# Kernel tuning notes

Measured on AMD Instinct MI355X. Metric: run time of the kernel, lower is better.

Reference implementation:

```python
import jax, jax.numpy as jnp
import numpy as np

N_NODES = 100000
N_EDGES = 1600000
IN_SIZE = 128
HIDDEN = 128
OUT_SIZE = 64


def setup_inputs() -> dict:
    key = jax.random.key(0)
    k = jax.random.split(key, 8)
    feat = jax.random.normal(k[0], (N_NODES, IN_SIZE), dtype=jnp.float32)
    src = jax.random.randint(k[1], (N_EDGES,), 0, N_NODES, dtype=jnp.int32)
    dst = jax.random.randint(k[2], (N_EDGES,), 0, N_NODES, dtype=jnp.int32)
    # fc_neigh weights for the two SAGEConv layers (stored as [in, out])
    W1 = jax.random.normal(k[3], (IN_SIZE, HIDDEN), dtype=jnp.float32) / np.sqrt(IN_SIZE)
    b1 = jnp.zeros((HIDDEN,), dtype=jnp.float32)
    W2 = jax.random.normal(k[4], (HIDDEN, OUT_SIZE), dtype=jnp.float32) / np.sqrt(HIDDEN)
    b2 = jnp.zeros((OUT_SIZE,), dtype=jnp.float32)
    return {"feat": feat, "W1": W1, "b1": b1, "W2": W2, "b2": b2,
            "src": src, "dst": dst}


def _sage_gcn(h, src, dst, W, b):
    # DGL SAGEConv with aggregator_type='gcn':
    #   neigh = segment_sum over incoming edges of src features
    #   h_neigh = (neigh + h_self) / (in_degree + 1)
    #   out = h_neigh @ W + b   (fc_self is not used for 'gcn')
    neigh = jax.ops.segment_sum(h[src], dst, num_segments=N_NODES)  # [N, d]
    deg = jax.ops.segment_sum(jnp.ones((src.shape[0],), dtype=h.dtype), dst,
                              num_segments=N_NODES)                 # [N]
    h_neigh = (neigh + h) / (deg + 1.0)[:, None]
    return h_neigh @ W + b


def reference(feat, W1, b1, W2, b2, src, dst):
    # dropout(p=0.0) is identity; activation between layers only
    h = _sage_gcn(feat, src, dst, W1, b1)
    h = jax.nn.relu(h)
    h = _sage_gcn(h, src, dst, W2, b2)
    return h
```

## Files before the change

### kernel.cpp

```cpp
#include <hip/hip_runtime.h>

#define NNODES 100000
#define NEDGES 1600000
#define BSHIFT 7
#define NB 782
#define CAP 2560
#define EBLOCKS 391
#define GEMM_BLOCKS 1563

typedef _Float16 f16;
typedef _Float16 v4h __attribute__((ext_vector_type(4)));
typedef _Float16 v8h __attribute__((ext_vector_type(8)));
typedef float v4f __attribute__((ext_vector_type(4)));

__global__ __launch_bounds__(256) void init_k(int* __restrict__ bcur,
                                              const float* __restrict__ W1,
                                              f16* __restrict__ W1t,
                                              const float* __restrict__ W2,
                                              f16* __restrict__ W2t) {
    int t = blockIdx.x * 256 + threadIdx.x;
    if (t < NB) bcur[t] = t * CAP;
    int u = t - 1024;
    if (u >= 0) {
        if (u < 128 * 128) {
            int k = u >> 7, n = u & 127;
            W1t[n * 128 + k] = (f16)W1[k * 128 + n];
        } else if (u < 128 * 128 + 128 * 64) {
            int v = u - 128 * 128;
            int k = v >> 6, n = v & 63;
            W2t[n * 128 + k] = (f16)W2[k * 64 + n];
        }
    }
}

__global__ __launch_bounds__(256) void scatter_gemm1(
    const int* __restrict__ src, const int* __restrict__ dst,
    int* __restrict__ bcur, int* __restrict__ ebuf,
    const float* __restrict__ feat, const f16* __restrict__ W1t,
    f16* __restrict__ z1) {
    constexpr int PITCH = 136;
    __shared__ __align__(16) char smem[128 * PITCH * 2];
    int tid = threadIdx.x;

    if (blockIdx.x < EBLOCKS) {
        int* h = (int*)smem;
        int* base_s = ((int*)smem) + 1024;
        for (int i = tid; i < NB; i += 256) h[i] = 0;
        __syncthreads();
        int base = blockIdx.x * 4096;
        int d[16], sv[16];
        for (int k = 0; k < 16; k++) {
            int e = base + k * 256 + tid;
            if (e < NEDGES) {
                d[k] = dst[e];
                sv[k] = src[e];
                atomicAdd(&h[d[k] >> BSHIFT], 1);
            } else {
                d[k] = -1;
            }
        }
        __syncthreads();
        for (int i = tid; i < NB; i += 256) {
            int c = h[i];
            if (c) base_s[i] = atomicAdd(&bcur[i], c);
            h[i] = 0;
        }
        __syncthreads();
        for (int k = 0; k < 16; k++) {
            if (d[k] >= 0) {
                int b = d[k] >> BSHIFT;
                int slot = atomicAdd(&h[b], 1);
                ebuf[base_s[b] + slot] = sv[k] | ((d[k] & 127) << 24);
            }
        }
        return;
    }

    f16* wlds = (f16*)smem;
    for (int c = tid; c < 128 * 16; c += 256) {
        int n = c >> 4;
        int kc = c & 15;
        *(v8h*)&wlds[n * PITCH + kc * 8] = *(const v8h*)&W1t[n * 128 + kc * 8];
    }
    __syncthreads();

    int wave = tid >> 6, lane = tid & 63, quad = lane >> 4, l16 = lane & 15;
    int m0 = (blockIdx.x - EBLOCKS) * 64 + wave * 16;
    if (m0 >= NNODES) return;

    v8h a[4];
    const float* arow = feat + (long)(m0 + l16) * 128 + quad * 8;
#pragma unroll
    for (int kb = 0; kb < 4; kb++) {
        float4 f0 = *(const float4*)(arow + kb * 32);
        float4 f1 = *(const float4*)(arow + kb * 32 + 4);
        v8h t = {(f16)f0.x, (f16)f0.y, (f16)f0.z, (f16)f0.w,
                 (f16)f1.x, (f16)f1.y, (f16)f1.z, (f16)f1.w};
        a[kb] = t;
    }

#pragma unroll
    for (int nt = 0; nt < 8; nt++) {
        v4f acc = {0.f, 0.f, 0.f, 0.f};
        const f16* brow = &wlds[(nt * 16 + l16) * PITCH + quad * 8];
#pragma unroll
        for (int kb = 0; kb < 4; kb++) {
            v8h b = *(const v8h*)(brow + kb * 32);
            acc = __builtin_amdgcn_mfma_f32_16x16x32_f16(a[kb], b, acc, 0, 0, 0);
        }
        int n = nt * 16 + l16;
#pragma unroll
        for (int r = 0; r < 4; r++)
            z1[(long)(m0 + quad * 4 + r) * 128 + n] = (f16)acc[r];
    }
}

__global__ __launch_bounds__(256) void fill_bucket(const int* __restrict__ ebuf,
                                                   const int* __restrict__ bcur,
                                                   int* __restrict__ begs,
                                                   int* __restrict__ ends,
                                                   int* __restrict__ csr) {
    __shared__ int lc[128];
    __shared__ int ls[256];
    int b = blockIdx.x;
    int tid = threadIdx.x;
    if (tid < 128) lc[tid] = 0;
    __syncthreads();
    int ebeg = b * CAP;
    int eend = bcur[b];
    for (int e = ebeg + tid; e < eend; e += 256)
        atomicAdd(&lc[((unsigned)ebuf[e]) >> 24], 1);
    __syncthreads();
    int cnt = (tid < 128) ? lc[tid] : 0;
    ls[tid] = cnt;
    __syncthreads();
    for (int off = 1; off < 256; off <<= 1) {
        int t = (tid >= off) ? ls[tid - off] : 0;
        __syncthreads();
        ls[tid] += t;
        __syncthreads();
    }
    int excl = ls[tid] - cnt;
    int node = (b << BSHIFT) + tid;
    if (tid < 128 && node < NNODES) {
        begs[node] = ebeg + excl;
        ends[node] = ebeg + excl + cnt;
    }
    if (tid < 128) { ls[tid] = excl; lc[tid] = 0; }
    __syncthreads();
    for (int e = ebeg + tid; e < eend; e += 256) {
        int p = ebuf[e];
        int dloc = ((unsigned)p) >> 24;
        int slot = atomicAdd(&lc[dloc], 1);
        csr[ebeg + ls[dloc] + slot] = p & 0xFFFFFF;
    }
}

__global__ __launch_bounds__(1024, 8) void gather128_gemm2(
    const f16* __restrict__ z,
    const int* __restrict__ begs, const int* __restrict__ ends,
    const int* __restrict__ csr,
    const float* __restrict__ b1,
    const f16* __restrict__ W2t,
    f16* __restrict__ z2)
{
    constexpr int PITCH = 136;
    __shared__ f16 w2lds[64 * PITCH];
    __shared__ f16 atile[64 * PITCH];
    int tid = threadIdx.x;

    {
        int n = tid >> 4, kc = tid & 15;
        *(v8h*)&w2lds[n * PITCH + kc * 8] = *(const v8h*)&W2t[n * 128 + kc * 8];
    }

    int wavei = tid >> 6;
    int lane = tid & 63;
    int sub = lane >> 4;
    int c = lane & 15;
    int lnode = wavei * 4 + sub;
    int node = blockIdx.x * 64 + lnode;

    int beg = 0, end = 0;
    if (node < NNODES) { beg = begs[node]; end = ends[node]; }

    const char* zb = (const char*)z;
    unsigned coff = (unsigned)c << 4;

    float af[8];
#pragma unroll
    for (int j = 0; j < 8; j++) af[j] = 0.f;

    if (node < NNODES) {
        v8h sv = *(const v8h*)(zb + ((unsigned)node << 8) + coff);
#pragma unroll
        for (int j = 0; j < 8; j++) af[j] = (float)sv[j];
    }

    int e = beg;
    while (__any(e < end)) {
        v8h u0 = {0,0,0,0,0,0,0,0}, u1 = {0,0,0,0,0,0,0,0};
        v8h u2 = {0,0,0,0,0,0,0,0}, u3 = {0,0,0,0,0,0,0,0};
        v8h u4 = {0,0,0,0,0,0,0,0}, u5 = {0,0,0,0,0,0,0,0};
        v8h u6 = {0,0,0,0,0,0,0,0}, u7 = {0,0,0,0,0,0,0,0};
        if (e     < end) u0 = *(const v8h*)(zb + (((unsigned)csr[e    ]) << 8) + coff);
        if (e + 1 < end) u1 = *(const v8h*)(zb + (((unsigned)csr[e + 1]) << 8) + coff);
        if (e + 2 < end) u2 = *(const v8h*)(zb + (((unsigned)csr[e + 2]) << 8) + coff);
        if (e + 3 < end) u3 = *(const v8h*)(zb + (((unsigned)csr[e + 3]) << 8) + coff);
        if (e + 4 < end) u4 = *(const v8h*)(zb + (((unsigned)csr[e + 4]) << 8) + coff);
        if (e + 5 < end) u5 = *(const v8h*)(zb + (((unsigned)csr[e + 5]) << 8) + coff);
        if (e + 6 < end) u6 = *(const v8h*)(zb + (((unsigned)csr[e + 6]) << 8) + coff);
        if (e + 7 < end) u7 = *(const v8h*)(zb + (((unsigned)csr[e + 7]) << 8) + coff);
        v8h s01 = u0 + u1, s23 = u2 + u3, s45 = u4 + u5, s67 = u6 + u7;
        v8h s03 = s01 + s23, s47 = s45 + s67;
        v8h s = s03 + s47;
#pragma unroll
        for (int j = 0; j < 8; j++) af[j] += (float)s[j];
        e += 8;
    }

    {
        float inv = 1.0f / (float)(end - beg + 1);
        float4 bb0 = ((const float4*)b1)[c * 2];
        float4 bb1 = ((const float4*)b1)[c * 2 + 1];
        v8h o = {(f16)fmaxf(af[0] * inv + bb0.x, 0.f),
                 (f16)fmaxf(af[1] * inv + bb0.y, 0.f),
                 (f16)fmaxf(af[2] * inv + bb0.z, 0.f),
                 (f16)fmaxf(af[3] * inv + bb0.w, 0.f),
                 (f16)fmaxf(af[4] * inv + bb1.x, 0.f),
                 (f16)fmaxf(af[5] * inv + bb1.y, 0.f),
                 (f16)fmaxf(af[6] * inv + bb1.z, 0.f),
                 (f16)fmaxf(af[7] * inv + bb1.w, 0.f)};
        *(v8h*)&atile[lnode * PITCH + c * 8] = o;
    }
    __syncthreads();

    {
        int wr = wavei >> 2, wc = wavei & 3;
        int quad = lane >> 4, l16 = lane & 15;
        const f16* arow = &atile[(wr * 16 + l16) * PITCH + quad * 8];
        const f16* brow = &w2lds[(wc * 16 + l16) * PITCH + quad * 8];
        v4f acc = {0.f, 0.f, 0.f, 0.f};
#pragma unroll
        for (int kb = 0; kb < 4; kb++) {
            v8h av = *(const v8h*)(arow + kb * 32);
            v8h bv = *(const v8h*)(brow + kb * 32);
            acc = __builtin_amdgcn_mfma_f32_16x16x32_f16(av, bv, acc, 0, 0, 0);
        }
        int n = wc * 16 + l16;
        int m0 = blockIdx.x * 64 + wr * 16;
#pragma unroll
        for (int r = 0; r < 4; r++) {
            int row = m0 + quad * 4 + r;
            if (row < NNODES) z2[(long)row * 64 + n] = (f16)acc[r];
        }
    }
}

__global__ __launch_bounds__(256, 8) void gather64(
    const f16* __restrict__ z, const int* __restrict__ begs,
    const int* __restrict__ ends, const int* __restrict__ csr,
    const float* __restrict__ bias, float4* __restrict__ out) {
    int tid = threadIdx.x;
    int lane = tid & 63;
    int c = lane & 7;
    int node = blockIdx.x * 32 + (tid >> 3);

    int beg = begs[node];
    int end = ends[node];

    const char* zb = (const char*)z;
    unsigned coff = (unsigned)c << 4;

    float af[8];
    {
        v8h sv = *(const v8h*)(zb + ((unsigned)node << 7) + coff);
#pragma unroll
        for (int j = 0; j < 8; j++) af[j] = (float)sv[j];
    }

    int e = beg;
    while (__any(e < end)) {
        v8h u0 = {0,0,0,0,0,0,0,0}, u1 = {0,0,0,0,0,0,0,0};
        v8h u2 = {0,0,0,0,0,0,0,0}, u3 = {0,0,0,0,0,0,0,0};
        v8h u4 = {0,0,0,0,0,0,0,0}, u5 = {0,0,0,0,0,0,0,0};
        v8h u6 = {0,0,0,0,0,0,0,0}, u7 = {0,0,0,0,0,0,0,0};
        if (e     < end) u0 = *(const v8h*)(zb + (((unsigned)csr[e    ]) << 7) + coff);
        if (e + 1 < end) u1 = *(const v8h*)(zb + (((unsigned)csr[e + 1]) << 7) + coff);
        if (e + 2 < end) u2 = *(const v8h*)(zb + (((unsigned)csr[e + 2]) << 7) + coff);
        if (e + 3 < end) u3 = *(const v8h*)(zb + (((unsigned)csr[e + 3]) << 7) + coff);
        if (e + 4 < end) u4 = *(const v8h*)(zb + (((unsigned)csr[e + 4]) << 7) + coff);
        if (e + 5 < end) u5 = *(const v8h*)(zb + (((unsigned)csr[e + 5]) << 7) + coff);
        if (e + 6 < end) u6 = *(const v8h*)(zb + (((unsigned)csr[e + 6]) << 7) + coff);
        if (e + 7 < end) u7 = *(const v8h*)(zb + (((unsigned)csr[e + 7]) << 7) + coff);
        v8h s01 = u0 + u1, s23 = u2 + u3, s45 = u4 + u5, s67 = u6 + u7;
        v8h s03 = s01 + s23, s47 = s45 + s67;
        v8h s = s03 + s47;
#pragma unroll
        for (int j = 0; j < 8; j++) af[j] += (float)s[j];
        e += 8;
    }

    {
        float inv = 1.0f / (float)(end - beg + 1);
        float4 b0 = ((const float4*)bias)[c * 2];
        float4 b1v = ((const float4*)bias)[c * 2 + 1];
        out[(long)node * 16 + c * 2] =
            make_float4(af[0] * inv + b0.x, af[1] * inv + b0.y,
                        af[2] * inv + b0.z, af[3] * inv + b0.w);
        out[(long)node * 16 + c * 2 + 1] =
            make_float4(af[4] * inv + b1v.x, af[5] * inv + b1v.y,
                        af[6] * inv + b1v.z, af[7] * inv + b1v.w);
    }
}

extern "C" void kernel_launch(void* const* d_in, const int* in_sizes, int n_in,
                              void* d_out, int out_size, void* d_ws, size_t ws_size,
                              hipStream_t stream) {
    const float* feat = (const float*)d_in[0];
    const float* W1   = (const float*)d_in[1];
    const float* b1   = (const float*)d_in[2];
    const float* W2   = (const float*)d_in[3];
    const float* b2   = (const float*)d_in[4];
    const int*   src  = (const int*)d_in[5];
    const int*   dst  = (const int*)d_in[6];
    float* out = (float*)d_out;

    char* ws = (char*)d_ws;
    int* bcur = (int*)(ws + 0x0000000);
    int* begs = (int*)(ws + 0x0001000);
    int* ends = (int*)(ws + 0x0063000);
    int* csr  = (int*)(ws + 0x00C5000);
    int* ebuf = (int*)(ws + 0x0870000);
    f16* z1   = (f16*)(ws + 0x1100000);
    f16* z2   = (f16*)(ws + 0x2A00000);
    f16* W1t  = (f16*)(ws + 0x3700000);
    f16* W2t  = (f16*)(ws + 0x3710000);

    init_k<<<100, 256, 0, stream>>>(bcur, W1, W1t, W2, W2t);

    scatter_gemm1<<<EBLOCKS + GEMM_BLOCKS, 256, 0, stream>>>(src, dst, bcur, ebuf,
                                                             feat, W1t, z1);

    fill_bucket<<<NB, 256, 0, stream>>>(ebuf, bcur, begs, ends, csr);

    gather128_gemm2<<<1563, 1024, 0, stream>>>(z1, begs, ends, csr, b1, W2t, z2);

    gather64<<<3125, 256, 0, stream>>>(z2, begs, ends, csr, b2, (float4*)out);
}
```

Measured before the change: 247.9 us.

## Quantize intermediate node features to per-row int8 with scales for gathers

The per-node projected features z1 and z2 are now stored as offset-uint8 values with a per-row float scale instead of fp16. The two neighbor-gather kernels dequantize on the fly with fma against the per-row scale and subtract the offset via a running scale sum. This halves the bytes fetched per gathered edge row in the memory-bound gather phases. In exchange it costs an extra scale load per edge, more ALU work, a shared-memory row-max reduction with an added barrier in the second GEMM, and a large loss of numerical precision that may exceed tolerance.

```diff
diff --git a/kernel.cpp b/kernel.cpp
--- a/kernel.cpp
+++ b/kernel.cpp
@@ -9,9 +9,19 @@
 #define GEMM_BLOCKS 1563
 
 typedef _Float16 f16;
-typedef _Float16 v4h __attribute__((ext_vector_type(4)));
 typedef _Float16 v8h __attribute__((ext_vector_type(8)));
 typedef float v4f __attribute__((ext_vector_type(4)));
+
+__device__ inline void acc8(float s, uint2 u, float* a) {
+    a[0] = fmaf(s, (float)(u.x & 0xFF), a[0]);
+    a[1] = fmaf(s, (float)((u.x >> 8) & 0xFF), a[1]);
+    a[2] = fmaf(s, (float)((u.x >> 16) & 0xFF), a[2]);
+    a[3] = fmaf(s, (float)(u.x >> 24), a[3]);
+    a[4] = fmaf(s, (float)(u.y & 0xFF), a[4]);
+    a[5] = fmaf(s, (float)((u.y >> 8) & 0xFF), a[5]);
+    a[6] = fmaf(s, (float)((u.y >> 16) & 0xFF), a[6]);
+    a[7] = fmaf(s, (float)(u.y >> 24), a[7]);
+}
 
 __global__ __launch_bounds__(256) void init_k(int* __restrict__ bcur,
                                               const float* __restrict__ W1,
@@ -37,7 +47,7 @@
     const int* __restrict__ src, const int* __restrict__ dst,
     int* __restrict__ bcur, int* __restrict__ ebuf,
     const float* __restrict__ feat, const f16* __restrict__ W1t,
-    f16* __restrict__ z1) {
+    unsigned char* __restrict__ z1, float* __restrict__ sc1) {
     constexpr int PITCH = 136;
     __shared__ __align__(16) char smem[128 * PITCH * 2];
     int tid = threadIdx.x;
@@ -99,19 +109,36 @@
         a[kb] = t;
     }
 
+    v4f acc[8];
 #pragma unroll
     for (int nt = 0; nt < 8; nt++) {
-        v4f acc = {0.f, 0.f, 0.f, 0.f};
+        v4f c4 = {0.f, 0.f, 0.f, 0.f};
         const f16* brow = &wlds[(nt * 16 + l16) * PITCH + quad * 8];
 #pragma unroll
         for (int kb = 0; kb < 4; kb++) {
             v8h b = *(const v8h*)(brow + kb * 32);
-            acc = __builtin_amdgcn_mfma_f32_16x16x32_f16(a[kb], b, acc, 0, 0, 0);
-        }
-        int n = nt * 16 + l16;
-#pragma unroll
-        for (int r = 0; r < 4; r++)
-            z1[(long)(m0 + quad * 4 + r) * 128 + n] = (f16)acc[r];
+            c4 = __builtin_amdgcn_mfma_f32_16x16x32_f16(a[kb], b, c4, 0, 0, 0);
+        }
+        acc[nt] = c4;
+    }
+
+#pragma unroll
+    for (int r = 0; r < 4; r++) {
+        float m = 0.f;
+#pragma unroll
+        for (int nt = 0; nt < 8; nt++) m = fmaxf(m, fabsf(acc[nt][r]));
+        m = fmaxf(m, __shfl_xor(m, 1));
+        m = fmaxf(m, __shfl_xor(m, 2));
+        m = fmaxf(m, __shfl_xor(m, 4));
+        m = fmaxf(m, __shfl_xor(m, 8));
+        int row = m0 + quad * 4 + r;
+        float rs = (m > 0.f) ? 127.f / m : 0.f;
+        if (l16 == 0) sc1[row] = (m > 0.f) ? m / 127.f : 0.f;
+#pragma unroll
+        for (int nt = 0; nt < 8; nt++) {
+            int qv = (int)rintf(acc[nt][r] * rs) + 128;
+            z1[(long)row * 128 + nt * 16 + l16] = (unsigned char)qv;
+        }
     }
 }
 
@@ -157,22 +184,26 @@
 }
 
 __global__ __launch_bounds__(1024, 8) void gather128_gemm2(
-    const f16* __restrict__ z,
+    const unsigned char* __restrict__ z,
+    const float* __restrict__ sc,
     const int* __restrict__ begs, const int* __restrict__ ends,
     const int* __restrict__ csr,
     const float* __restrict__ b1,
     const f16* __restrict__ W2t,
-    f16* __restrict__ z2)
+    unsigned char* __restrict__ z2,
+    float* __restrict__ sc2)
 {
     constexpr int PITCH = 136;
     __shared__ f16 w2lds[64 * PITCH];
     __shared__ f16 atile[64 * PITCH];
+    __shared__ int rmax[64];
     int tid = threadIdx.x;
 
     {
         int n = tid >> 4, kc = tid & 15;
         *(v8h*)&w2lds[n * PITCH + kc * 8] = *(const v8h*)&W2t[n * 128 + kc * 8];
     }
+    if (tid < 64) rmax[tid] = 0;
 
     int wavei = tid >> 6;
     int lane = tid & 63;
@@ -184,53 +215,55 @@
     int beg = 0, end = 0;
     if (node < NNODES) { beg = begs[node]; end = ends[node]; }
 
-    const char* zb = (const char*)z;
-    unsigned coff = (unsigned)c << 4;
-
-    float af[8];
-#pragma unroll
-    for (int j = 0; j < 8; j++) af[j] = 0.f;
+    unsigned coff = (unsigned)c << 3;
+
+    float a[8];
+#pragma unroll
+    for (int j = 0; j < 8; j++) a[j] = 0.f;
+    float ssum = 0.f;
 
     if (node < NNODES) {
-        v8h sv = *(const v8h*)(zb + ((unsigned)node << 8) + coff);
-#pragma unroll
-        for (int j = 0; j < 8; j++) af[j] = (float)sv[j];
+        float s = sc[node];
+        uint2 u = *(const uint2*)(z + (((unsigned)node) << 7) + coff);
+        ssum += s;
+        acc8(s, u, a);
     }
 
     int e = beg;
     while (__any(e < end)) {
-        v8h u0 = {0,0,0,0,0,0,0,0}, u1 = {0,0,0,0,0,0,0,0};
-        v8h u2 = {0,0,0,0,0,0,0,0}, u3 = {0,0,0,0,0,0,0,0};
-        v8h u4 = {0,0,0,0,0,0,0,0}, u5 = {0,0,0,0,0,0,0,0};
-        v8h u6 = {0,0,0,0,0,0,0,0}, u7 = {0,0,0,0,0,0,0,0};
-        if (e     < end) u0 = *(const v8h*)(zb + (((unsigned)csr[e    ]) << 8) + coff);
-        if (e + 1 < end) u1 = *(const v8h*)(zb + (((unsigned)csr[e + 1]) << 8) + coff);
-        if (e + 2 < end) u2 = *(const v8h*)(zb + (((unsigned)csr[e + 2]) << 8) + coff);
-        if (e + 3 < end) u3 = *(const v8h*)(zb + (((unsigned)csr[e + 3]) << 8) + coff);
-        if (e + 4 < end) u4 = *(const v8h*)(zb + (((unsigned)csr[e + 4]) << 8) + coff);
-        if (e + 5 < end) u5 = *(const v8h*)(zb + (((unsigned)csr[e + 5]) << 8) + coff);
-        if (e + 6 < end) u6 = *(const v8h*)(zb + (((unsigned)csr[e + 6]) << 8) + coff);
-        if (e + 7 < end) u7 = *(const v8h*)(zb + (((unsigned)csr[e + 7]) << 8) + coff);
-        v8h s01 = u0 + u1, s23 = u2 + u3, s45 = u4 + u5, s67 = u6 + u7;
-        v8h s03 = s01 + s23, s47 = s45 + s67;
-        v8h s = s03 + s47;
-#pragma unroll
-        for (int j = 0; j < 8; j++) af[j] += (float)s[j];
+        float s0 = 0.f, s1 = 0.f, s2 = 0.f, s3 = 0.f;
+        float s4 = 0.f, s5 = 0.f, s6 = 0.f, s7 = 0.f;
+        uint2 u0 = make_uint2(0, 0), u1 = make_uint2(0, 0);
+        uint2 u2 = make_uint2(0, 0), u3 = make_uint2(0, 0);
+        uint2 u4 = make_uint2(0, 0), u5 = make_uint2(0, 0);
+        uint2 u6 = make_uint2(0, 0), u7 = make_uint2(0, 0);
+        if (e     < end) { int i = csr[e    ]; s0 = sc[i]; u0 = *(const uint2*)(z + (((unsigned)i) << 7) + coff); }
+        if (e + 1 < end) { int i = csr[e + 1]; s1 = sc[i]; u1 = *(const uint2*)(z + (((unsigned)i) << 7) + coff); }
+        if (e + 2 < end) { int i = csr[e + 2]; s2 = sc[i]; u2 = *(const uint2*)(z + (((unsigned)i) << 7) + coff); }
+        if (e + 3 < end) { int i = csr[e + 3]; s3 = sc[i]; u3 = *(const uint2*)(z + (((unsigned)i) << 7) + coff); }
+        if (e + 4 < end) { int i = csr[e + 4]; s4 = sc[i]; u4 = *(const uint2*)(z + (((unsigned)i) << 7) + coff); }
+        if (e + 5 < end) { int i = csr[e + 5]; s5 = sc[i]; u5 = *(const uint2*)(z + (((unsigned)i) << 7) + coff); }
+        if (e + 6 < end) { int i = csr[e + 6]; s6 = sc[i]; u6 = *(const uint2*)(z + (((unsigned)i) << 7) + coff); }
+        if (e + 7 < end) { int i = csr[e + 7]; s7 = sc[i]; u7 = *(const uint2*)(z + (((unsigned)i) << 7) + coff); }
+        ssum += ((s0 + s1) + (s2 + s3)) + ((s4 + s5) + (s6 + s7));
+        acc8(s0, u0, a); acc8(s1, u1, a); acc8(s2, u2, a); acc8(s3, u3, a);
+        acc8(s4, u4, a); acc8(s5, u5, a); acc8(s6, u6, a); acc8(s7, u7, a);
         e += 8;
     }
 
     {
+        float base = 128.f * ssum;
         float inv = 1.0f / (float)(end - beg + 1);
         float4 bb0 = ((const float4*)b1)[c * 2];
         float4 bb1 = ((const float4*)b1)[c * 2 + 1];
-        v8h o = {(f16)fmaxf(af[0] * inv + bb0.x, 0.f),
-                 (f16)fmaxf(af[1] * inv + bb0.y, 0.f),
-                 (f16)fmaxf(af[2] * inv + bb0.z, 0.f),
-                 (f16)fmaxf(af[3] * inv + bb0.w, 0.f),
-                 (f16)fmaxf(af[4] * inv + bb1.x, 0.f),
-                 (f16)fmaxf(af[5] * inv + bb1.y, 0.f),
-                 (f16)fmaxf(af[6] * inv + bb1.z, 0.f),
-                 (f16)fmaxf(af[7] * inv + bb1.w, 0.f)};
+        v8h o = {(f16)fmaxf((a[0] - base) * inv + bb0.x, 0.f),
+                 (f16)fmaxf((a[1] - base) * inv + bb0.y, 0.f),
+                 (f16)fmaxf((a[2] - base) * inv + bb0.z, 0.f),
+                 (f16)fmaxf((a[3] - base) * inv + bb0.w, 0.f),
+                 (f16)fmaxf((a[4] - base) * inv + bb1.x, 0.f),
+                 (f16)fmaxf((a[5] - base) * inv + bb1.y, 0.f),
+                 (f16)fmaxf((a[6] - base) * inv + bb1.z, 0.f),
+                 (f16)fmaxf((a[7] - base) * inv + bb1.w, 0.f)};
         *(v8h*)&atile[lnode * PITCH + c * 8] = o;
     }
     __syncthreads();
@@ -247,19 +280,35 @@
             v8h bv = *(const v8h*)(brow + kb * 32);
             acc = __builtin_amdgcn_mfma_f32_16x16x32_f16(av, bv, acc, 0, 0, 0);
         }
-        int n = wc * 16 + l16;
-        int m0 = blockIdx.x * 64 + wr * 16;
 #pragma unroll
         for (int r = 0; r < 4; r++) {
-            int row = m0 + quad * 4 + r;
-            if (row < NNODES) z2[(long)row * 64 + n] = (f16)acc[r];
+            float m = fabsf(acc[r]);
+            m = fmaxf(m, __shfl_xor(m, 1));
+            m = fmaxf(m, __shfl_xor(m, 2));
+            m = fmaxf(m, __shfl_xor(m, 4));
+            m = fmaxf(m, __shfl_xor(m, 8));
+            if (l16 == 0) atomicMax(&rmax[wr * 16 + quad * 4 + r], __float_as_int(m));
+        }
+        __syncthreads();
+#pragma unroll
+        for (int r = 0; r < 4; r++) {
+            int lrow = wr * 16 + quad * 4 + r;
+            int row = blockIdx.x * 64 + lrow;
+            if (row < NNODES) {
+                float m = __int_as_float(rmax[lrow]);
+                float rs = (m > 0.f) ? 127.f / m : 0.f;
+                int qv = (int)rintf(acc[r] * rs) + 128;
+                z2[(long)row * 64 + wc * 16 + l16] = (unsigned char)qv;
+                if (l16 == 0 && wc == 0) sc2[row] = (m > 0.f) ? m / 127.f : 0.f;
+            }
         }
     }
 }
 
 __global__ __launch_bounds__(256, 8) void gather64(
-    const f16* __restrict__ z, const int* __restrict__ begs,
-    const int* __restrict__ ends, const int* __restrict__ csr,
+    const unsigned char* __restrict__ z, const float* __restrict__ sc,
+    const int* __restrict__ begs, const int* __restrict__ ends,
+    const int* __restrict__ csr,
     const float* __restrict__ bias, float4* __restrict__ out) {
     int tid = threadIdx.x;
     int lane = tid & 63;
@@ -269,48 +318,53 @@
     int beg = begs[node];
     int end = ends[node];
 
-    const char* zb = (const char*)z;
-    unsigned coff = (unsigned)c << 4;
-
-    float af[8];
+    unsigned coff = (unsigned)c << 3;
+
+    float a[8];
+#pragma unroll
+    for (int j = 0; j < 8; j++) a[j] = 0.f;
+    float ssum = 0.f;
+
     {
-        v8h sv = *(const v8h*)(zb + ((unsigned)node << 7) + coff);
-#pragma unroll
-        for (int j = 0; j < 8; j++) af[j] = (float)sv[j];
+        float s = sc[node];
+        uint2 u = *(const uint2*)(z + (((unsigned)node) << 6) + coff);
+        ssum += s;
+        acc8(s, u, a);
     }
 
     int e = beg;
     while (__any(e < end)) {
-        v8h u0 = {0,0,0,0,0,0,0,0}, u1 = {0,0,0,0,0,0,0,0};
-        v8h u2 = {0,0,0,0,0,0,0,0}, u3 = {0,0,0,0,0,0,0,0};
-        v8h u4 = {0,0,0,0,0,0,0,0}, u5 = {0,0,0,0,0,0,0,0};
-        v8h u6 = {0,0,0,0,0,0,0,0}, u7 = {0,0,0,0,0,0,0,0};
-        if (e     < end) u0 = *(const v8h*)(zb + (((unsigned)csr[e    ]) << 7) + coff);
-        if (e + 1 < end) u1 = *(const v8h*)(zb + (((unsigned)csr[e + 1]) << 7) + coff);
-        if (e + 2 < end) u2 = *(const v8h*)(zb + (((unsigned)csr[e + 2]) << 7) + coff);
-        if (e + 3 < end) u3 = *(const v8h*)(zb + (((unsigned)csr[e + 3]) << 7) + coff);
-        if (e + 4 < end) u4 = *(const v8h*)(zb + (((unsigned)csr[e + 4]) << 7) + coff);
-        if (e + 5 < end) u5 = *(const v8h*)(zb + (((unsigned)csr[e + 5]) << 7) + coff);
-        if (e + 6 < end) u6 = *(const v8h*)(zb + (((unsigned)csr[e + 6]) << 7) + coff);
-        if (e + 7 < end) u7 = *(const v8h*)(zb + (((unsigned)csr[e + 7]) << 7) + coff);
-        v8h s01 = u0 + u1, s23 = u2 + u3, s45 = u4 + u5, s67 = u6 + u7;
-        v8h s03 = s01 + s23, s47 = s45 + s67;
-        v8h s = s03 + s47;
-#pragma unroll
-        for (int j = 0; j < 8; j++) af[j] += (float)s[j];
+        float s0 = 0.f, s1 = 0.f, s2 = 0.f, s3 = 0.f;
+        float s4 = 0.f, s5 = 0.f, s6 = 0.f, s7 = 0.f;
+        uint2 u0 = make_uint2(0, 0), u1 = make_uint2(0, 0);
+        uint2 u2 = make_uint2(0, 0), u3 = make_uint2(0, 0);
+        uint2 u4 = make_uint2(0, 0), u5 = make_uint2(0, 0);
+        uint2 u6 = make_uint2(0, 0), u7 = make_uint2(0, 0);
+        if (e     < end) { int i = csr[e    ]; s0 = sc[i]; u0 = *(const uint2*)(z + (((unsigned)i) << 6) + coff); }
+        if (e + 1 < end) { int i = csr[e + 1]; s1 = sc[i]; u1 = *(const uint2*)(z + (((unsigned)i) << 6) + coff); }
+        if (e + 2 < end) { int i = csr[e + 2]; s2 = sc[i]; u2 = *(const uint2*)(z + (((unsigned)i) << 6) + coff); }
+        if (e + 3 < end) { int i = csr[e + 3]; s3 = sc[i]; u3 = *(const uint2*)(z + (((unsigned)i) << 6) + coff); }
+        if (e + 4 < end) { int i = csr[e + 4]; s4 = sc[i]; u4 = *(const uint2*)(z + (((unsigned)i) << 6) + coff); }
+        if (e + 5 < end) { int i = csr[e + 5]; s5 = sc[i]; u5 = *(const uint2*)(z + (((unsigned)i) << 6) + coff); }
+        if (e + 6 < end) { int i = csr[e + 6]; s6 = sc[i]; u6 = *(const uint2*)(z + (((unsigned)i) << 6) + coff); }
+        if (e + 7 < end) { int i = csr[e + 7]; s7 = sc[i]; u7 = *(const uint2*)(z + (((unsigned)i) << 6) + coff); }
+        ssum += ((s0 + s1) + (s2 + s3)) + ((s4 + s5) + (s6 + s7));
+        acc8(s0, u0, a); acc8(s1, u1, a); acc8(s2, u2, a); acc8(s3, u3, a);
+        acc8(s4, u4, a); acc8(s5, u5, a); acc8(s6, u6, a); acc8(s7, u7, a);
         e += 8;
     }
 
     {
+        float base = 128.f * ssum;
         float inv = 1.0f / (float)(end - beg + 1);
         float4 b0 = ((const float4*)bias)[c * 2];
         float4 b1v = ((const float4*)bias)[c * 2 + 1];
         out[(long)node * 16 + c * 2] =
-            make_float4(af[0] * inv + b0.x, af[1] * inv + b0.y,
-                        af[2] * inv + b0.z, af[3] * inv + b0.w);
+            make_float4((a[0] - base) * inv + b0.x, (a[1] - base) * inv + b0.y,
+                        (a[2] - base) * inv + b0.z, (a[3] - base) * inv + b0.w);
         out[(long)node * 16 + c * 2 + 1] =
-            make_float4(af[4] * inv + b1v.x, af[5] * inv + b1v.y,
-                        af[6] * inv + b1v.z, af[7] * inv + b1v.w);
+            make_float4((a[4] - base) * inv + b1v.x, (a[5] - base) * inv + b1v.y,
+                        (a[6] - base) * inv + b1v.z, (a[7] - base) * inv + b1v.w);
     }
 }
 
@@ -332,19 +386,22 @@
     int* ends = (int*)(ws + 0x0063000);
     int* csr  = (int*)(ws + 0x00C5000);
     int* ebuf = (int*)(ws + 0x0870000);
-    f16* z1   = (f16*)(ws + 0x1100000);
-    f16* z2   = (f16*)(ws + 0x2A00000);
+    unsigned char* z1 = (unsigned char*)(ws + 0x1100000);
+    float* sc1 = (float*)(ws + 0x2000000);
+    unsigned char* z2 = (unsigned char*)(ws + 0x2A00000);
+    float* sc2 = (float*)(ws + 0x3100000);
     f16* W1t  = (f16*)(ws + 0x3700000);
     f16* W2t  = (f16*)(ws + 0x3710000);
 
     init_k<<<100, 256, 0, stream>>>(bcur, W1, W1t, W2, W2t);
 
     scatter_gemm1<<<EBLOCKS + GEMM_BLOCKS, 256, 0, stream>>>(src, dst, bcur, ebuf,
-                                                             feat, W1t, z1);
+                                                             feat, W1t, z1, sc1);
 
     fill_bucket<<<NB, 256, 0, stream>>>(ebuf, bcur, begs, ends, csr);
 
-    gather128_gemm2<<<1563, 1024, 0, stream>>>(z1, begs, ends, csr, b1, W2t, z2);
-
-    gather64<<<3125, 256, 0, stream>>>(z2, begs, ends, csr, b2, (float4*)out);
-}
+    gather128_gemm2<<<1563, 1024, 0, stream>>>(z1, sc1, begs, ends, csr, b1, W2t,
+                                               z2, sc2);
+
+    gather64<<<3125, 256, 0, stream>>>(z2, sc2, begs, ends, csr, b2, (float4*)out);
+}
```

After: 249.6 us. Within noise of the previous version (+0.7%).
